# Optimization experiments

Hardware: AMD Instinct MI355X
Metric: run time of the kernel (lower is better)

Reference implementation:

```python
import jax, jax.numpy as jnp
import numpy as np
from jax import lax

B, T, D, R, V = 128, 8, 2048, 4, 512

def setup_inputs() -> dict:
    key = jax.random.key(0)
    k0, k1, k2, k3, k4 = jax.random.split(key, 5)
    # scales chosen so the TT products stay within fp32 range (see notes)
    input_embs = jax.random.normal(k0, (B, T, D), dtype=jnp.float32) * 0.1
    label_ids = jax.random.randint(k1, (B, T), 0, V)
    w_alpha = jax.random.normal(k2, (D, R), dtype=jnp.float32) * 0.04
    w_beta = jax.random.normal(k3, (D, R), dtype=jnp.float32) * 0.04
    w_vocab = jax.random.normal(k4, (D, V * R * R), dtype=jnp.float32) * 0.04
    return {"input_embs": input_embs, "label_ids": label_ids,
            "w_alpha": w_alpha, "w_beta": w_beta, "w_vocab": w_vocab}

def _tt_loss(input_embs, w_alpha, w_beta, w_vocab, label_ids):
    b, t, d = input_embs.shape
    flat = input_embs.reshape(-1, d)                    # [B*T, D]
    alpha = jnp.abs((flat @ w_alpha).reshape(b, t, R).mean(1))   # [B, R]
    beta = jnp.abs((flat @ w_beta).reshape(b, t, R).mean(1))     # [B, R]
    core = jnp.abs((flat @ w_vocab).reshape(b, t, R, V, R).mean(1))  # [B, R, V, R]

    # --- _select: gather per-position R x R cores and chain-multiply ---
    core_v = core.transpose(0, 2, 1, 3)                 # [B, V, R, R]
    sel = jnp.take_along_axis(core_v, label_ids[:, :, None, None], axis=1)  # [B, T, R, R]
    sel_t = jnp.swapaxes(sel, 0, 1)                     # [T, B, R, R]

    def chain(carry, m):
        return jnp.einsum('bik,bkj->bij', carry, m), None
    res, _ = lax.scan(chain, sel_t[0], sel_t[1:])       # [B, R, R]
    u = jnp.einsum('bi,bij,bj->b', alpha, res, beta)    # unnormalized probs [B]

    # --- normalization constant: marg^(T+1) contracted with alpha/beta ---
    marg = core.sum(2)                                  # [B, R, R]

    def pow_step(c, _):
        return jnp.einsum('bik,bkj->bij', c, marg), None
    zmat, _ = lax.scan(pow_step, marg, None, length=t)  # marg^(t+1)
    z = jnp.einsum('bi,bij,bj->b', alpha, zmat, beta)

    loss = -jnp.log(u / z)
    return loss.mean()

def reference(input_embs, label_ids, w_alpha, w_beta, w_vocab):
    return _tt_loss(input_embs, w_alpha, w_beta, w_vocab, label_ids)
```

## Files before the change

### kernel.cpp

```cpp
#include <hip/hip_runtime.h>
#include <math.h>

#define BB 128
#define TT 8
#define DD 2048
#define RR 4
#define VV 512

typedef __attribute__((ext_vector_type(8))) short short8;
typedef __attribute__((ext_vector_type(4))) float v4f;

__global__ __launch_bounds__(256) void phaseA(const float* __restrict__ inp,
                                              const float* __restrict__ w_alpha,
                                              const float* __restrict__ w_beta,
                                              unsigned short* __restrict__ fmb,
                                              float* __restrict__ alphaP,
                                              float* __restrict__ betaP,
                                              float* __restrict__ marg) {
    int bid = blockIdx.x;
    int b = bid >> 1, half = bid & 1;
    int tid = threadIdx.x;
    if (bid == 0) {
#pragma unroll
        for (int e = 0; e < 8; ++e) marg[e * 256 + tid] = 0.f;
    }
    const float* base = inp + (size_t)b * TT * DD;
    float pa[4] = {0.f, 0.f, 0.f, 0.f};
    float pb[4] = {0.f, 0.f, 0.f, 0.f};
#pragma unroll
    for (int i = 0; i < 4; ++i) {
        int d = half * 1024 + i * 256 + tid;
        float s = 0.f;
#pragma unroll
        for (int t = 0; t < TT; ++t) s += base[t * DD + d];
        float v = s * (1.0f / TT);
        union { float f; unsigned u; } cv; cv.f = v;
        unsigned r = cv.u + 0x7fffu + ((cv.u >> 16) & 1u);
        fmb[b * DD + d] = (unsigned short)(r >> 16);
        float4 wa = *(const float4*)(w_alpha + d * 4);
        float4 wb = *(const float4*)(w_beta + d * 4);
        pa[0] += v * wa.x; pa[1] += v * wa.y; pa[2] += v * wa.z; pa[3] += v * wa.w;
        pb[0] += v * wb.x; pb[1] += v * wb.y; pb[2] += v * wb.z; pb[3] += v * wb.w;
    }
#pragma unroll
    for (int r = 0; r < 4; ++r) {
        for (int m = 1; m < 64; m <<= 1) {
            pa[r] += __shfl_xor(pa[r], m);
            pb[r] += __shfl_xor(pb[r], m);
        }
    }
    __shared__ float red[4][8];
    if ((tid & 63) == 0) {
        int w = tid >> 6;
#pragma unroll
        for (int r = 0; r < 4; ++r) { red[w][r] = pa[r]; red[w][4 + r] = pb[r]; }
    }
    __syncthreads();
    if (tid < 8) {
        float s = red[0][tid] + red[1][tid] + red[2][tid] + red[3][tid];
        if (tid < 4) alphaP[(half * BB + b) * 4 + tid] = s;
        else         betaP[(half * BB + b) * 4 + (tid - 4)] = s;
    }
}

__global__ __launch_bounds__(512) void phaseB(const unsigned short* __restrict__ fmb,
                                              const float* __restrict__ wv,
                                              const int* __restrict__ labels,
                                              float* __restrict__ marg,
                                              float* __restrict__ sel) {
    __shared__ float xch[4][4][64][4];
    __shared__ int slab[BB * TT];

    const int tid = threadIdx.x;
    slab[tid] = labels[tid];
    slab[tid + 512] = labels[tid + 512];

    const int nb = blockIdx.x;
    const int w = tid >> 6, lane = tid & 63;
    const int m15 = lane & 15, q = lane >> 4;
    const int ch = w & 1;
    const int rh = (w >> 1) & 1;
    const int kh = w >> 2;
    const int colg = nb * 32 + ch * 16 + m15;

    v4f acc[4];
#pragma unroll
    for (int t = 0; t < 4; ++t) acc[t] = (v4f){0.f, 0.f, 0.f, 0.f};

    const float* wvp = wv + (size_t)(kh * 1024 + q * 8) * 8192 + colg;
    const unsigned short* ap = fmb + (size_t)(rh * 64 + m15) * DD + kh * 1024 + q * 8;

#pragma unroll 2
    for (int kc = 0; kc < 32; ++kc) {
        float f[8];
#pragma unroll
        for (int j = 0; j < 8; ++j) f[j] = wvp[(size_t)j * 8192];
        short8 bf;
        unsigned* bu = (unsigned*)&bf;
#pragma unroll
        for (int p = 0; p < 4; ++p) {
            union { float ff; unsigned u; } x0, x1;
            x0.ff = f[2 * p]; x1.ff = f[2 * p + 1];
            bu[p] = (x0.u >> 16) | (x1.u & 0xffff0000u);
        }
#pragma unroll
        for (int tile = 0; tile < 4; ++tile) {
            short8 af = *(const short8*)(ap + tile * 16 * DD);
            acc[tile] = __builtin_amdgcn_mfma_f32_16x16x32_bf16(af, bf, acc[tile], 0, 0, 0);
        }
        wvp += (size_t)32 * 8192;
        ap += 32;
    }

    if (kh == 1) {
#pragma unroll
        for (int tile = 0; tile < 4; ++tile)
            *(v4f*)&xch[w - 4][tile][lane][0] = acc[tile];
    }
    __syncthreads();
    if (kh == 1) return;
#pragma unroll
    for (int tile = 0; tile < 4; ++tile)
        acc[tile] += *(const v4f*)&xch[w][tile][lane][0];

    const int i4 = (nb >> 6) * 4;
    const int jj = m15 & 3;
    const int v = (nb & 63) * 8 + ch * 4 + (m15 >> 2);
#pragma unroll
    for (int tile = 0; tile < 4; ++tile) {
#pragma unroll
        for (int r = 0; r < 4; ++r) {
            int m = rh * 64 + tile * 16 + q * 4 + r;
            float a = fabsf(acc[tile][r]);
            float s = a + __shfl_xor(a, 4);
            s += __shfl_xor(s, 8);
            if (m15 < 4) atomicAdd(&marg[m * 16 + i4 + m15], s);
#pragma unroll
            for (int t = 0; t < TT; ++t) {
                if (slab[m * 8 + t] == v) sel[(m * 8 + t) * 16 + i4 + jj] = a;
            }
        }
    }
}

__global__ __launch_bounds__(128) void phaseD(const float* __restrict__ alphaP,
                                              const float* __restrict__ betaP,
                                              const float* __restrict__ marg,
                                              const float* __restrict__ sel,
                                              float* __restrict__ out) {
    int b = threadIdx.x;
    float alpha[4], beta[4];
#pragma unroll
    for (int r = 0; r < 4; ++r) {
        alpha[r] = fabsf(alphaP[b * 4 + r] + alphaP[512 + b * 4 + r]);
        beta[r]  = fabsf(betaP[b * 4 + r] + betaP[512 + b * 4 + r]);
    }
    const float* sb = sel + b * TT * 16;
    float res[16], tmp[16], mm[16], zm[16];
#pragma unroll
    for (int ee = 0; ee < 16; ++ee) res[ee] = sb[ee];
    for (int t = 1; t < TT; ++t) {
        const float* m = sb + t * 16;
#pragma unroll
        for (int i = 0; i < 4; ++i)
#pragma unroll
            for (int jj = 0; jj < 4; ++jj) {
                float s = 0.f;
#pragma unroll
                for (int k = 0; k < 4; ++k) s += res[i * 4 + k] * m[k * 4 + jj];
                tmp[i * 4 + jj] = s;
            }
#pragma unroll
        for (int ee = 0; ee < 16; ++ee) res[ee] = tmp[ee];
    }
#pragma unroll
    for (int ee = 0; ee < 16; ++ee) { mm[ee] = marg[b * 16 + ee]; zm[ee] = mm[ee]; }
    for (int st = 0; st < TT; ++st) {
#pragma unroll
        for (int i = 0; i < 4; ++i)
#pragma unroll
            for (int jj = 0; jj < 4; ++jj) {
                float s = 0.f;
#pragma unroll
                for (int k = 0; k < 4; ++k) s += zm[i * 4 + k] * mm[k * 4 + jj];
                tmp[i * 4 + jj] = s;
            }
#pragma unroll
        for (int ee = 0; ee < 16; ++ee) zm[ee] = tmp[ee];
    }
    float u = 0.f, z = 0.f;
#pragma unroll
    for (int i = 0; i < 4; ++i) {
#pragma unroll
        for (int jj = 0; jj < 4; ++jj) {
            u += alpha[i] * res[i * 4 + jj] * beta[jj];
            z += alpha[i] * zm[i * 4 + jj] * beta[jj];
        }
    }
    float loss = logf(z) - logf(u);
    __shared__ float red[128];
    red[b] = loss;
    __syncthreads();
    for (int off = 64; off >= 1; off >>= 1) {
        if (b < off) red[b] += red[b + off];
        __syncthreads();
    }
    if (b == 0) out[0] = red[0] * (1.0f / BB);
}

extern "C" void kernel_launch(void* const* d_in, const int* in_sizes, int n_in,
                              void* d_out, int out_size, void* d_ws, size_t ws_size,
                              hipStream_t stream) {
    const float* inp     = (const float*)d_in[0];
    const int*   labels  = (const int*)d_in[1];
    const float* w_alpha = (const float*)d_in[2];
    const float* w_beta  = (const float*)d_in[3];
    const float* wv      = (const float*)d_in[4];
    float* out = (float*)d_out;

    float* ws     = (float*)d_ws;
    float* alphaP = ws;
    float* betaP  = ws + 1024;
    float* marg   = ws + 2048;
    float* sel    = ws + 4096;
    unsigned short* fmb = (unsigned short*)(ws + 20480);

    phaseA<<<256, 256, 0, stream>>>(inp, w_alpha, w_beta, fmb, alphaP, betaP, marg);
    phaseB<<<256, 512, 0, stream>>>(fmb, wv, labels, marg, sel);
    phaseD<<<1, 128, 0, stream>>>(alphaP, betaP, marg, sel, out);
}
```

Measured before the change: 151.0 us.

## Stage w_vocab tiles via global_load_lds double-buffering with 512 narrower blocks

The vocab GEMM kernel now streams 128x16 fp32 tiles of w_vocab into LDS with async global_load_lds in a double-buffered loop, and prefetches activation fragments into registers. Work is split into 512 blocks of 256 threads, each owning 16 columns and all K, which removes the split-K LDS reduction. The aim is to turn strided per-lane global loads of the 64 MB weight into coalesced 16-byte row loads and to overlap the next tile's load with MFMA work. The cost is an extra barrier per chunk and strided LDS reads for fp32-to-bf16 conversion.

```diff
diff --git a/kernel.cpp b/kernel.cpp
--- a/kernel.cpp
+++ b/kernel.cpp
@@ -9,6 +9,11 @@
 
 typedef __attribute__((ext_vector_type(8))) short short8;
 typedef __attribute__((ext_vector_type(4))) float v4f;
+
+#define GLL(g, l)                                                              \
+    __builtin_amdgcn_global_load_lds(                                          \
+        (const __attribute__((address_space(1))) unsigned int*)(g),            \
+        (__attribute__((address_space(3))) unsigned int*)(l), 16, 0, 0)
 
 __global__ __launch_bounds__(256) void phaseA(const float* __restrict__ inp,
                                               const float* __restrict__ w_alpha,
@@ -63,74 +68,86 @@
     }
 }
 
-__global__ __launch_bounds__(512) void phaseB(const unsigned short* __restrict__ fmb,
-                                              const float* __restrict__ wv,
-                                              const int* __restrict__ labels,
-                                              float* __restrict__ marg,
-                                              float* __restrict__ sel) {
-    __shared__ float xch[4][4][64][4];
+__global__ __launch_bounds__(256, 2) void phaseB(const unsigned short* __restrict__ fmb,
+                                                 const float* __restrict__ wv,
+                                                 const int* __restrict__ labels,
+                                                 float* __restrict__ marg,
+                                                 float* __restrict__ sel) {
+    __shared__ float Wt[2][128][16];
     __shared__ int slab[BB * TT];
 
     const int tid = threadIdx.x;
+    const int nb = blockIdx.x;
+    const int col0 = nb * 16;
+
     slab[tid] = labels[tid];
+    slab[tid + 256] = labels[tid + 256];
     slab[tid + 512] = labels[tid + 512];
-
-    const int nb = blockIdx.x;
+    slab[tid + 768] = labels[tid + 768];
+
     const int w = tid >> 6, lane = tid & 63;
     const int m15 = lane & 15, q = lane >> 4;
-    const int ch = w & 1;
-    const int rh = (w >> 1) & 1;
-    const int kh = w >> 2;
-    const int colg = nb * 32 + ch * 16 + m15;
-
-    v4f acc[4];
-#pragma unroll
-    for (int t = 0; t < 4; ++t) acc[t] = (v4f){0.f, 0.f, 0.f, 0.f};
-
-    const float* wvp = wv + (size_t)(kh * 1024 + q * 8) * 8192 + colg;
-    const unsigned short* ap = fmb + (size_t)(rh * 64 + m15) * DD + kh * 1024 + q * 8;
-
-#pragma unroll 2
-    for (int kc = 0; kc < 32; ++kc) {
-        float f[8];
-#pragma unroll
-        for (int j = 0; j < 8; ++j) f[j] = wvp[(size_t)j * 8192];
-        short8 bf;
-        unsigned* bu = (unsigned*)&bf;
-#pragma unroll
-        for (int p = 0; p < 4; ++p) {
-            union { float ff; unsigned u; } x0, x1;
-            x0.ff = f[2 * p]; x1.ff = f[2 * p + 1];
-            bu[p] = (x0.u >> 16) | (x1.u & 0xffff0000u);
-        }
-#pragma unroll
-        for (int tile = 0; tile < 4; ++tile) {
-            short8 af = *(const short8*)(ap + tile * 16 * DD);
-            acc[tile] = __builtin_amdgcn_mfma_f32_16x16x32_bf16(af, bf, acc[tile], 0, 0, 0);
-        }
-        wvp += (size_t)32 * 8192;
-        ap += 32;
-    }
-
-    if (kh == 1) {
-#pragma unroll
-        for (int tile = 0; tile < 4; ++tile)
-            *(v4f*)&xch[w - 4][tile][lane][0] = acc[tile];
+
+    const int srow = w * 16 + (lane >> 2);
+    const float* gsb = wv + (size_t)srow * 8192 + col0 + (lane & 3) * 4;
+
+    const unsigned short* ap = fmb + (size_t)(w * 32 + m15) * DD + q * 8;
+
+    v4f acc[2];
+    acc[0] = (v4f){0.f, 0.f, 0.f, 0.f};
+    acc[1] = (v4f){0.f, 0.f, 0.f, 0.f};
+    short8 afr[2][2][4];
+
+    GLL(gsb, &Wt[0][w * 16][0]);
+    GLL(gsb + (size_t)64 * 8192, &Wt[0][64 + w * 16][0]);
+#pragma unroll
+    for (int ks = 0; ks < 4; ++ks) {
+        afr[0][0][ks] = *(const short8*)(ap + ks * 32);
+        afr[0][1][ks] = *(const short8*)(ap + 16 * DD + ks * 32);
     }
     __syncthreads();
-    if (kh == 1) return;
-#pragma unroll
-    for (int tile = 0; tile < 4; ++tile)
-        acc[tile] += *(const v4f*)&xch[w][tile][lane][0];
-
-    const int i4 = (nb >> 6) * 4;
+
+#pragma unroll 1
+    for (int c = 0; c < 16; ++c) {
+        const int cur = c & 1;
+        if (c < 15) {
+            const float* gs = gsb + (size_t)(c + 1) * 128 * 8192;
+            GLL(gs, &Wt[1 - cur][w * 16][0]);
+            GLL(gs + (size_t)64 * 8192, &Wt[1 - cur][64 + w * 16][0]);
+            const unsigned short* an = ap + (c + 1) * 128;
+#pragma unroll
+            for (int ks = 0; ks < 4; ++ks) {
+                afr[1 - cur][0][ks] = *(const short8*)(an + ks * 32);
+                afr[1 - cur][1][ks] = *(const short8*)(an + 16 * DD + ks * 32);
+            }
+        }
+#pragma unroll
+        for (int ks = 0; ks < 4; ++ks) {
+            float f[8];
+#pragma unroll
+            for (int j = 0; j < 8; ++j) f[j] = Wt[cur][ks * 32 + q * 8 + j][m15];
+            short8 bf;
+            unsigned* bu = (unsigned*)&bf;
+#pragma unroll
+            for (int p = 0; p < 4; ++p) {
+                union { float ff; unsigned u; } x0, x1;
+                x0.ff = f[2 * p]; x1.ff = f[2 * p + 1];
+                bu[p] = (x0.u >> 16) | (x1.u & 0xffff0000u);
+            }
+            acc[0] = __builtin_amdgcn_mfma_f32_16x16x32_bf16(afr[cur][0][ks], bf, acc[0], 0, 0, 0);
+            acc[1] = __builtin_amdgcn_mfma_f32_16x16x32_bf16(afr[cur][1][ks], bf, acc[1], 0, 0, 0);
+        }
+        __syncthreads();
+    }
+
+    const int i4 = (nb >> 7) * 4;
     const int jj = m15 & 3;
-    const int v = (nb & 63) * 8 + ch * 4 + (m15 >> 2);
-#pragma unroll
-    for (int tile = 0; tile < 4; ++tile) {
+    const int v = (nb & 127) * 4 + (m15 >> 2);
+#pragma unroll
+    for (int tile = 0; tile < 2; ++tile) {
 #pragma unroll
         for (int r = 0; r < 4; ++r) {
-            int m = rh * 64 + tile * 16 + q * 4 + r;
+            int m = w * 32 + tile * 16 + q * 4 + r;
             float a = fabsf(acc[tile][r]);
             float s = a + __shfl_xor(a, 4);
             s += __shfl_xor(s, 8);
@@ -226,6 +243,6 @@
     unsigned short* fmb = (unsigned short*)(ws + 20480);
 
     phaseA<<<256, 256, 0, stream>>>(inp, w_alpha, w_beta, fmb, alphaP, betaP, marg);
-    phaseB<<<256, 512, 0, stream>>>(fmb, wv, labels, marg, sel);
+    phaseB<<<512, 256, 0, stream>>>(fmb, wv, labels, marg, sel);
     phaseD<<<1, 128, 0, stream>>>(alphaP, betaP, marg, sel, out);
 }
```

After: 224.6 us. +48.8%, slower.
